# Kernel tuning notes

Hardware: AMD Instinct MI355X
Metric: run time of the kernel (lower is better)

The kernel has to match this reference:

```python
import jax, jax.numpy as jnp
import numpy as np

N = 100_000   # nodes
E = 3_200_000 # edges (avg degree 32)

def _glorot(k, shape):
    fan_in, fan_out = shape
    lim = float(np.sqrt(6.0 / (fan_in + fan_out)))
    return jax.random.uniform(k, shape, jnp.float32, -lim, lim)

def setup_inputs() -> dict:
    key = jax.random.key(0)
    ks = jax.random.split(key, 8)
    x = jax.random.normal(ks[0], (N, 3), dtype=jnp.float32)
    edge_index = jax.random.randint(ks[1], (2, E), 0, N, dtype=jnp.int32)
    choices = jax.random.bernoulli(ks[2], 0.5, (N,))
    W1 = _glorot(ks[3], (3, 16));  b1 = jnp.zeros((16,), jnp.float32)
    W2 = _glorot(ks[4], (16, 16)); b2 = jnp.zeros((16,), jnp.float32)
    W3 = _glorot(ks[5], (16, 1));  b3 = jnp.zeros((1,), jnp.float32)
    fc_w = _glorot(ks[6], (16, 1)); fc_b = jnp.zeros((1,), jnp.float32)
    return dict(x=x, edge_index=edge_index, choices=choices,
                W1=W1, b1=b1, W2=W2, b2=b2, W3=W3, b3=b3,
                fc_w=fc_w, fc_b=fc_b)

def reference(x, edge_index, choices, W1, b1, W2, b2, W3, b3, fc_w, fc_b):
    row, col = edge_index[0], edge_index[1]  # source -> target
    # improved=True GCN norm: self-loop weight 2, deg = in_degree + 2
    deg = jax.ops.segment_sum(jnp.ones((E,), x.dtype), col, num_segments=N) + 2.0
    dinv = jax.lax.rsqrt(deg)                    # [N]
    enorm = dinv[row] * dinv[col]                # [E] edge normalization
    self_norm = 2.0 * dinv * dinv                # [N] self-loop term

    def gcn(h, W, b):
        h = h @ W                                # [N, F_out]
        agg = jax.ops.segment_sum(h[row] * enorm[:, None], col, num_segments=N)
        return agg + self_norm[:, None] * h + b

    h = jax.nn.relu(gcn(x, W1, b1))
    h = jax.nn.relu(gcn(h, W2, b2))
    c = gcn(h, W3, b3)[:, 0]                     # [N] per-node logit
    # masked softmax over chosen nodes (torch masked_select + softmax,
    # expressed with static shape: non-chosen entries get probability 0)
    logits = jnp.where(choices, c, -jnp.inf)
    choice = jax.nn.softmax(logits, axis=0)      # [N]
    # global_mean_pool with a single graph = mean over all nodes
    v = jnp.mean(h, axis=0, keepdims=True)       # [1, 16]
    value = v @ fc_w + fc_b                      # [1, 1]
    return choice, value
```

## Files before the change

### kernel.cpp

```cpp
#include <hip/hip_runtime.h>
#include <hip/hip_fp16.h>
#include <math.h>

#define BLK 256


#define BSH 8
#define NB 512
#define CAP 10240
#define SCAP 12288
#define EB 8192
#define BINTH 1024

__device__ inline float4 load_h4(const __half* base, int node, int sub) {
    const uint2* p = reinterpret_cast<const uint2*>(base + ((size_t)node << 4)) + sub;
    uint2 u = *p;
    union { unsigned u; __half2 h; } a, b;
    a.u = u.x; b.u = u.y;
    float2 fa = __half22float2(a.h), fb = __half22float2(b.h);
    return make_float4(fa.x, fa.y, fb.x, fb.y);
}

__device__ inline void store_h4(__half* base, int node, int sub, float4 v) {
    union { unsigned u; __half2 h; } a, b;
    a.h = __floats2half2_rn(v.x, v.y);
    b.h = __floats2half2_rn(v.z, v.w);
    uint2 u; u.x = a.u; u.y = b.u;
    *(reinterpret_cast<uint2*>(base + ((size_t)node << 4)) + sub) = u;
}

__device__ inline float3 load_xs(const __half* xs, int node) {
    uint2 u = *reinterpret_cast<const uint2*>(xs + ((size_t)node << 2));
    union { unsigned u; __half2 h; } a, b;
    a.u = u.x; b.u = u.y;
    float2 fa = __half22float2(a.h), fb = __half22float2(b.h);
    return make_float3(fa.x, fa.y, fb.x);
}

__global__ void k_init(int* __restrict__ gcur, float* __restrict__ scal) {
    int t = threadIdx.x;
    gcur[t] = 0;
    if (t < 18) scal[t] = 0.f;
}

__global__ void __launch_bounds__(BINTH) k_bin(const int* __restrict__ row,
                                               const int* __restrict__ col,
                                               int* __restrict__ gcur,
                                               int* __restrict__ packed, int E) {
    __shared__ int stage[EB];
    __shared__ unsigned short sbuk[EB];
    __shared__ int hist[NB];
    __shared__ int lscan[NB];
    __shared__ int cur[NB];
    __shared__ int gbase[NB];
    int tid = threadIdx.x;
    int base = blockIdx.x * EB;
    int cnt = min(EB, E - base);

    if (tid < NB) hist[tid] = 0;
    __syncthreads();
    for (int j = tid; j < cnt; j += BINTH) {
        int c = __builtin_nontemporal_load(col + base + j);
        atomicAdd(&hist[c >> BSH], 1);
    }
    __syncthreads();
    if (tid < NB) lscan[tid] = hist[tid];
    __syncthreads();
    for (int d = 1; d < NB; d <<= 1) {
        int t = (tid < NB && tid >= d) ? lscan[tid - d] : 0;
        __syncthreads();
        if (tid < NB && tid >= d) lscan[tid] += t;
        __syncthreads();
    }
    if (tid < NB) {
        int ex = lscan[tid] - hist[tid];
        lscan[tid] = ex;
        cur[tid] = ex;
    }
    __syncthreads();
    for (int j = tid; j < cnt; j += BINTH) {
        int c = __builtin_nontemporal_load(col + base + j);
        int r = __builtin_nontemporal_load(row + base + j);
        int b = c >> BSH;
        int p = atomicAdd(&cur[b], 1);
        stage[p] = (r << BSH) | (c & ((1 << BSH) - 1));
        sbuk[p] = (unsigned short)b;
    }
    __syncthreads();
    if (tid < NB && hist[tid] > 0)
        gbase[tid] = tid * CAP + atomicAdd(&gcur[tid], hist[tid]);
    __syncthreads();
    for (int j = tid; j < cnt; j += BINTH) {
        int b = sbuk[j];
        int pos = gbase[b] + (j - lscan[b]);
        packed[pos] = stage[j];
    }
}

__global__ void __launch_bounds__(BLK) k_place(const int* __restrict__ packed,
                                               const int* __restrict__ bcnt,
                                               const float* __restrict__ x,
                                               int* __restrict__ degi,
                                               int* __restrict__ offs,
                                               float* __restrict__ dinv,
                                               __half* __restrict__ xs,
                                               int* __restrict__ srcs, int n) {
    __shared__ int cnt[256];
    __shared__ int lcur[256];
    __shared__ int ssum[256];
    __shared__ int stg[SCAP];
    int tid = threadIdx.x;
    int b = blockIdx.x;
    int nb0 = b << BSH;
    cnt[tid] = 0;
    __syncthreads();
    int ecnt = bcnt[b];
    const int* pk = packed + (size_t)b * CAP;
    for (int j = tid; j < ecnt; j += BLK)
        atomicAdd(&cnt[pk[j] & 255], 1);
    __syncthreads();
    int c = cnt[tid];
    int pl = (c + 7) & ~7;
    ssum[tid] = pl;
    __syncthreads();
    for (int d = 1; d < 256; d <<= 1) {
        int t = (tid >= d) ? ssum[tid - d] : 0;
        __syncthreads();
        if (tid >= d) ssum[tid] += t;
        __syncthreads();
    }
    int Arel = ssum[tid] - pl;
    lcur[tid] = Arel;
    int A = b * SCAP + Arel;
    int valid = min(n - nb0, 256);
    int i = nb0 + tid;
    if (tid < valid) {
        degi[i] = pl;
        offs[i] = A;
        float di = rsqrtf((float)c + 2.0f);
        dinv[i] = di;
        float x0 = x[i * 3 + 0], x1 = x[i * 3 + 1], x2 = x[i * 3 + 2];
        union { unsigned u; __half2 h; } a2, b2;
        a2.h = __floats2half2_rn(di * x0, di * x1);
        b2.h = __floats2half2_rn(di * x2, 0.f);
        uint2 u; u.x = a2.u; u.y = b2.u;
        *reinterpret_cast<uint2*>(xs + ((size_t)i << 2)) = u;
        for (int k = c; k < pl; k++) stg[Arel + k] = n;
    }
    if (b == 0 && tid == 0) {
        uint2 z; z.x = 0u; z.y = 0u;
        *reinterpret_cast<uint2*>(xs + ((size_t)n << 2)) = z;
    }
    __syncthreads();
    for (int j = tid; j < ecnt; j += BLK) {
        int v = pk[j];
        int slot = atomicAdd(&lcur[v & 255], 1);
        stg[slot] = v >> BSH;
    }
    __syncthreads();
    int total = ssum[255];
    int gb = b * SCAP;
    for (int j = tid; j < total; j += BLK)
        srcs[gb + j] = stg[j];
}

__global__ void __launch_bounds__(BLK) k_agg1(const __half* __restrict__ xs,
                                              const int* __restrict__ offs,
                                              const int* __restrict__ degi,
                                              const int* __restrict__ srcs,
                                              const float* __restrict__ dinv,
                                              const float* __restrict__ b1,
                                              const float* __restrict__ W1,
                                              const float* __restrict__ W2,
                                              __half* __restrict__ hwsB, int n) {
    __shared__ float w1[48];
    __shared__ float w2[256];
    __shared__ float bb[16];
    __shared__ float hbuf[64][17];
    int tid = threadIdx.x;
    w2[tid] = W2[tid];
    if (tid < 48) w1[tid] = W1[tid];
    if (tid < 16) bb[tid] = b1[tid];
    if (blockIdx.x == 0 && tid < 8)
        reinterpret_cast<unsigned*>(hwsB + ((size_t)n << 4))[tid] = 0u;
    __syncthreads();
    int t = tid >> 2, sub = tid & 3;
    int i = blockIdx.x * 64 + t;
    bool act = (i < n);
    int A  = act ? offs[i] : 0;
    int pl = act ? degi[i] : 0;
    int o = 4 * sub;
    int clamp = max(pl - 4, 0);
    float ax0 = 0.f, ay0 = 0.f, az0 = 0.f;
    float ax1 = 0.f, ay1 = 0.f, az1 = 0.f;
    for (int j = 0; j < pl; j += 32) {
        int i0 = j + o;
        int i1 = j + 16 + o;
        int ja = min(i0, clamp);
        int jb = min(i1, clamp);
        int4 sa = *reinterpret_cast<const int4*>(srcs + A + ja);
        int4 sb = *reinterpret_cast<const int4*>(srcs + A + jb);
        if (i0 >= pl) sa = make_int4(n, n, n, n);
        if (i1 >= pl) sb = make_int4(n, n, n, n);
        float3 qa0 = load_xs(xs, sa.x);
        float3 qa1 = load_xs(xs, sa.y);
        float3 qa2 = load_xs(xs, sa.z);
        float3 qa3 = load_xs(xs, sa.w);
        float3 qb0 = load_xs(xs, sb.x);
        float3 qb1 = load_xs(xs, sb.y);
        float3 qb2 = load_xs(xs, sb.z);
        float3 qb3 = load_xs(xs, sb.w);
        ax0 += qa0.x + qa1.x + qa2.x + qa3.x;
        ay0 += qa0.y + qa1.y + qa2.y + qa3.y;
        az0 += qa0.z + qa1.z + qa2.z + qa3.z;
        ax1 += qb0.x + qb1.x + qb2.x + qb3.x;
        ay1 += qb0.y + qb1.y + qb2.y + qb3.y;
        az1 += qb0.z + qb1.z + qb2.z + qb3.z;
    }
    float ax = ax0 + ax1, ay = ay0 + ay1, az = az0 + az1;
    ax += __shfl_xor(ax, 1); ay += __shfl_xor(ay, 1); az += __shfl_xor(az, 1);
    ax += __shfl_xor(ax, 2); ay += __shfl_xor(ay, 2); az += __shfl_xor(az, 2);
    float di = 0.f;
    if (act) {
        di = dinv[i];
        float3 s = load_xs(xs, i);
        float axs = ax + 2.f * s.x, ays = ay + 2.f * s.y, azs = az + 2.f * s.z;
#pragma unroll
        for (int k = 0; k < 4; k++) {
            int f = sub * 4 + k;
            float hv = di * (axs * w1[f] + ays * w1[16 + f] + azs * w1[32 + f]) + bb[f];
            hbuf[t][f] = fmaxf(hv, 0.f);
        }
    }
    __syncthreads();
    if (act) {
        const float* hn = hbuf[t];
        float s0 = 0.f, s1 = 0.f, s2 = 0.f, s3 = 0.f;
#pragma unroll
        for (int f = 0; f < 16; f++) {
            float hv = hn[f];
            const float4 wq = *(const float4*)&w2[f * 16 + sub * 4];
            s0 += hv * wq.x; s1 += hv * wq.y; s2 += hv * wq.z; s3 += hv * wq.w;
        }
        store_h4(hwsB, i, sub, make_float4(di * s0, di * s1, di * s2, di * s3));
    }
}

__global__ void __launch_bounds__(BLK) k_agg2(const __half* __restrict__ hwsB,
                                              const int* __restrict__ offs,
                                              const int* __restrict__ degi,
                                              const int* __restrict__ srcs,
                                              const float* __restrict__ dinv,
                                              const float* __restrict__ b2,
                                              const float* __restrict__ W3,
                                              float* __restrict__ hws3,
                                              float* __restrict__ pool, int n) {
    __shared__ float w3[16];
    __shared__ float bb[16];
    __shared__ float lp[16];
    int tid = threadIdx.x;
    if (tid < 16) { w3[tid] = W3[tid]; bb[tid] = b2[tid]; lp[tid] = 0.f; }
    if (blockIdx.x == 0 && tid == 0) hws3[n] = 0.f;
    __syncthreads();
    int t = tid >> 2, sub = tid & 3;
    int i = blockIdx.x * 64 + t;
    bool act = (i < n);
    float di = act ? dinv[i] : 0.f;
    int A  = act ? offs[i] : 0;
    int pl = act ? degi[i] : 0;
    float4 z4 = make_float4(0.f, 0.f, 0.f, 0.f);
    float4 s = act ? load_h4(hwsB, i, sub) : z4;
    float4 acc0 = make_float4(2.f * s.x, 2.f * s.y, 2.f * s.z, 2.f * s.w);
    float4 acc1 = z4, acc2 = z4, acc3 = z4;
    int clamp8 = max(pl - 8, 0);
    for (int j = 0; j < pl; j += 16) {
        int j1 = j + 8;
        int jb = min(j1, clamp8);
        int4 sa0 = *reinterpret_cast<const int4*>(srcs + A + j);
        int4 sa1 = *reinterpret_cast<const int4*>(srcs + A + j + 4);
        int4 sb0 = *reinterpret_cast<const int4*>(srcs + A + jb);
        int4 sb1 = *reinterpret_cast<const int4*>(srcs + A + jb + 4);
        if (j1 >= pl) { sb0 = make_int4(n, n, n, n); sb1 = sb0; }
        float4 qa0 = load_h4(hwsB, sa0.x, sub);
        float4 qa1 = load_h4(hwsB, sa0.y, sub);
        float4 qa2 = load_h4(hwsB, sa0.z, sub);
        float4 qa3 = load_h4(hwsB, sa0.w, sub);
        float4 qa4 = load_h4(hwsB, sa1.x, sub);
        float4 qa5 = load_h4(hwsB, sa1.y, sub);
        float4 qa6 = load_h4(hwsB, sa1.z, sub);
        float4 qa7 = load_h4(hwsB, sa1.w, sub);
        float4 qb0 = load_h4(hwsB, sb0.x, sub);
        float4 qb1 = load_h4(hwsB, sb0.y, sub);
        float4 qb2 = load_h4(hwsB, sb0.z, sub);
        float4 qb3 = load_h4(hwsB, sb0.w, sub);
        float4 qb4 = load_h4(hwsB, sb1.x, sub);
        float4 qb5 = load_h4(hwsB, sb1.y, sub);
        float4 qb6 = load_h4(hwsB, sb1.z, sub);
        float4 qb7 = load_h4(hwsB, sb1.w, sub);
        acc0.x += qa0.x + qa2.x + qa4.x + qa6.x;
        acc0.y += qa0.y + qa2.y + qa4.y + qa6.y;
        acc0.z += qa0.z + qa2.z + qa4.z + qa6.z;
        acc0.w += qa0.w + qa2.w + qa4.w + qa6.w;
        acc1.x += qa1.x + qa3.x + qa5.x + qa7.x;
        acc1.y += qa1.y + qa3.y + qa5.y + qa7.y;
        acc1.z += qa1.z + qa3.z + qa5.z + qa7.z;
        acc1.w += qa1.w + qa3.w + qa5.w + qa7.w;
        acc2.x += qb0.x + qb2.x + qb4.x + qb6.x;
        acc2.y += qb0.y + qb2.y + qb4.y + qb6.y;
        acc2.z += qb0.z + qb2.z + qb4.z + qb6.z;
        acc2.w += qb0.w + qb2.w + qb4.w + qb6.w;
        acc3.x += qb1.x + qb3.x + qb5.x + qb7.x;
        acc3.y += qb1.y + qb3.y + qb5.y + qb7.y;
        acc3.z += qb1.z + qb3.z + qb5.z + qb7.z;
        acc3.w += qb1.w + qb3.w + qb5.w + qb7.w;
    }
    acc0.x += acc1.x + acc2.x + acc3.x;
    acc0.y += acc1.y + acc2.y + acc3.y;
    acc0.z += acc1.z + acc2.z + acc3.z;
    acc0.w += acc1.w + acc2.w + acc3.w;
    float4 hA = z4;
    if (act) {
        hA.x = fmaxf(di * acc0.x + bb[sub * 4 + 0], 0.f);
        hA.y = fmaxf(di * acc0.y + bb[sub * 4 + 1], 0.f);
        hA.z = fmaxf(di * acc0.z + bb[sub * 4 + 2], 0.f);
        hA.w = fmaxf(di * acc0.w + bb[sub * 4 + 3], 0.f);
    }
    float pA = hA.x * w3[sub * 4 + 0] + hA.y * w3[sub * 4 + 1]
             + hA.z * w3[sub * 4 + 2] + hA.w * w3[sub * 4 + 3];
    pA += __shfl_xor(pA, 1); pA += __shfl_xor(pA, 2);
    if (sub == 0 && act) hws3[i] = di * pA;
    float4 hp = hA;
#pragma unroll
    for (int m = 4; m < 64; m <<= 1) {
        hp.x += __shfl_xor(hp.x, m);
        hp.y += __shfl_xor(hp.y, m);
        hp.z += __shfl_xor(hp.z, m);
        hp.w += __shfl_xor(hp.w, m);
    }
    if ((tid & 63) < 4) {
        atomicAdd(&lp[sub * 4 + 0], hp.x);
        atomicAdd(&lp[sub * 4 + 1], hp.y);
        atomicAdd(&lp[sub * 4 + 2], hp.z);
        atomicAdd(&lp[sub * 4 + 3], hp.w);
    }
    __syncthreads();
    if (tid < 16) atomicAdd(&pool[tid], lp[tid]);
}

__global__ void __launch_bounds__(BLK) k_agg3(const float* __restrict__ hws3,
                                              const int* __restrict__ offs,
                                              const int* __restrict__ degi,
                                              const int* __restrict__ srcs,
                                              const float* __restrict__ dinv,
                                              const float* __restrict__ b3,
                                              const int* __restrict__ choices,
                                              float* __restrict__ cbuf,
                                              float* __restrict__ bmax,
                                              float* __restrict__ bsum, int n) {
    __shared__ float red[BLK];
    int tid = threadIdx.x;
    int nl = tid >> 2, sub = tid & 3;
    int iA = blockIdx.x * 128 + nl;
    int iB = iA + 64;
    bool actA = (iA < n), actB = (iB < n);
    int AA = actA ? offs[iA] : 0;
    int AB = actB ? offs[iB] : 0;
    int plA = actA ? degi[iA] : 0;
    int plB = actB ? degi[iB] : 0;
    float sA0 = 0.f, sA1 = 0.f, sB0 = 0.f, sB1 = 0.f;
    int plM = max(plA, plB);
    for (int j = 8 * sub; j < plM; j += 32) {
        int ja = min(j, max(plA - 8, 0));
        int jb = min(j, max(plB - 8, 0));
        int4 sa0 = *reinterpret_cast<const int4*>(srcs + AA + ja);
        int4 sa1 = *reinterpret_cast<const int4*>(srcs + AA + ja + 4);
        int4 sb0 = *reinterpret_cast<const int4*>(srcs + AB + jb);
        int4 sb1 = *reinterpret_cast<const int4*>(srcs + AB + jb + 4);
        if (j >= plA) { sa0 = make_int4(n, n, n, n); sa1 = sa0; }
        if (j >= plB) { sb0 = make_int4(n, n, n, n); sb1 = sb0; }
        sA0 += hws3[sa0.x] + hws3[sa0.z] + hws3[sa1.x] + hws3[sa1.z];
        sA1 += hws3[sa0.y] + hws3[sa0.w] + hws3[sa1.y] + hws3[sa1.w];
        sB0 += hws3[sb0.x] + hws3[sb0.z] + hws3[sb1.x] + hws3[sb1.z];
        sB1 += hws3[sb0.y] + hws3[sb0.w] + hws3[sb1.y] + hws3[sb1.w];
    }
    float sA = sA0 + sA1, sB = sB0 + sB1;
    sA += __shfl_xor(sA, 1); sA += __shfl_xor(sA, 2);
    sB += __shfl_xor(sB, 1); sB += __shfl_xor(sB, 2);
    float lA = -INFINITY, lB = -INFINITY;
    if (sub == 0) {
        if (actA) {
            float c = dinv[iA] * (sA + 2.f * hws3[iA]) + b3[0];
            cbuf[iA] = c;
            if (choices[iA] != 0) lA = c;
        }
        if (actB) {
            float c = dinv[iB] * (sB + 2.f * hws3[iB]) + b3[0];
            cbuf[iB] = c;
            if (choices[iB] != 0) lB = c;
        }
    }
    red[tid] = fmaxf(lA, lB);
    __syncthreads();
    for (int d = BLK / 2; d > 0; d >>= 1) {
        if (tid < d) red[tid] = fmaxf(red[tid], red[tid + d]);
        __syncthreads();
    }
    float bm = red[0];
    __syncthreads();
    float es = 0.f;
    if (lA > -INFINITY) es += expf(lA - bm);
    if (lB > -INFINITY) es += expf(lB - bm);
    red[tid] = es;
    __syncthreads();
    for (int d = BLK / 2; d > 0; d >>= 1) {
        if (tid < d) red[tid] += red[tid + d];
        __syncthreads();
    }
    if (tid == 0) { bmax[blockIdx.x] = bm; bsum[blockIdx.x] = red[0]; }
}

__global__ void __launch_bounds__(BLK) k_final(const float* __restrict__ cbuf,
                                               const int* __restrict__ choices,
                                               const float* __restrict__ bmax,
                                               const float* __restrict__ bsum,
                                               const float* __restrict__ pool,
                                               const float* __restrict__ fcw,
                                               const float* __restrict__ fcb,
                                               float* __restrict__ out,
                                               int nblk, int n) {
    __shared__ float red[BLK];
    __shared__ float MS[2];
    int tid = threadIdx.x;
    float m = -INFINITY;
    for (int i = tid; i < nblk; i += BLK) m = fmaxf(m, bmax[i]);
    red[tid] = m;
    __syncthreads();
    for (int d = BLK / 2; d > 0; d >>= 1) {
        if (tid < d) red[tid] = fmaxf(red[tid], red[tid + d]);
        __syncthreads();
    }
    float M = red[0];
    __syncthreads();
    float s = 0.f;
    for (int i = tid; i < nblk; i += BLK) {
        float bm = bmax[i];
        if (bm > -INFINITY) s += bsum[i] * expf(bm - M);
    }
    red[tid] = s;
    __syncthreads();
    for (int d = BLK / 2; d > 0; d >>= 1) {
        if (tid < d) red[tid] += red[tid + d];
        __syncthreads();
    }
    if (tid == 0) { MS[0] = M; MS[1] = red[0]; }
    __syncthreads();
    float Mv = MS[0], Sv = MS[1];
    int i = blockIdx.x * BLK + tid;
    if (i < n) {
        float p = 0.0f;
        if (choices[i] != 0) p = expf(cbuf[i] - Mv) / Sv;
        out[i] = p;
    }
    if (blockIdx.x == 0 && tid == 0) {
        float invn = 1.0f / (float)n;
        float v = 0.0f;
#pragma unroll
        for (int f = 0; f < 16; f++) v += (pool[f] * invn) * fcw[f];
        out[n] = v + fcb[0];
    }
}

extern "C" void kernel_launch(void* const* d_in, const int* in_sizes, int n_in,
                              void* d_out, int out_size, void* d_ws, size_t ws_size,
                              hipStream_t stream) {
    const float* x       = (const float*)d_in[0];
    const int*   ei      = (const int*)d_in[1];
    const int*   choices = (const int*)d_in[2];
    const float* W1 = (const float*)d_in[3];
    const float* b1 = (const float*)d_in[4];
    const float* W2 = (const float*)d_in[5];
    const float* b2 = (const float*)d_in[6];
    const float* W3 = (const float*)d_in[7];
    const float* b3 = (const float*)d_in[8];
    const float* fcw = (const float*)d_in[9];
    const float* fcb = (const float*)d_in[10];
    float* out = (float*)d_out;

    int n = in_sizes[0] / 3;
    int E = in_sizes[1] / 2;
    const int* row = ei;
    const int* col = ei + E;

    int nblkN = (n + BLK - 1) / BLK;
    int nblk64 = (n + 63) / 64;
    int nblk128 = (n + 127) / 128;
    int nbuck = (n + (1 << BSH) - 1) >> BSH;
    int nblkBin = (E + EB - 1) / EB;

    char* ws = (char*)d_ws;
    size_t o = 0;
    auto alloc = [&](size_t bytes) { char* p = ws + o; o += (bytes + 15) & ~(size_t)15; return p; };
    int*   degi   = (int*)  alloc((size_t)n * 4);
    int*   offs   = (int*)  alloc((size_t)n * 4);
    float* dinv   = (float*)alloc((size_t)n * 4);
    float* hws3   = (float*)alloc((size_t)(n + 1) * 4);
    float* cbuf   = (float*)alloc((size_t)n * 4);
    float* bmax   = (float*)alloc(8192);
    float* bsum   = (float*)alloc(8192);
    int*   gcur   = (int*)  alloc(NB * 4);
    float* scal   = (float*)alloc(256);
    float* pool   = scal + 1;
    __half* xs    = (__half*)alloc((size_t)(n + 1) * 4 * 2);
    size_t hw_bytes = (size_t)(n + 1) * 16 * 2;
    size_t pk_bytes = (size_t)NB * CAP * 4;
    char*  blob   = alloc(hw_bytes > pk_bytes ? hw_bytes : pk_bytes);
    int*    packed = (int*)blob;
    __half* hwsB   = (__half*)blob;
    int*   srcs   = (int*)  alloc((size_t)NB * SCAP * 4);
    (void)ws_size;

    k_init<<<1, NB, 0, stream>>>(gcur, scal);
    k_bin<<<nblkBin, BINTH, 0, stream>>>(row, col, gcur, packed, E);
    k_place<<<nbuck, BLK, 0, stream>>>(packed, gcur, x, degi, offs, dinv, xs, srcs, n);

    k_agg1<<<nblk64, BLK, 0, stream>>>(xs, offs, degi, srcs, dinv, b1, W1, W2, hwsB, n);
    k_agg2<<<nblk64, BLK, 0, stream>>>(hwsB, offs, degi, srcs, dinv, b2, W3, hws3, pool, n);
    k_agg3<<<nblk128, BLK, 0, stream>>>(hws3, offs, degi, srcs, dinv, b3, choices, cbuf, bmax, bsum, n);

    k_final<<<nblkN, BLK, 0, stream>>>(cbuf, choices, bmax, bsum, pool, fcw, fcb, out, nblk128, n);
}
```

Measured before the change: 210.5 us.

## Sort nodes by padded degree within buckets to balance aggregation wavefronts

In the placement kernel, each 256-node bucket builds a permutation that groups nodes by padded degree class using a small shared-memory counting sort. The three aggregation kernels read node ids through this permutation, so wavefronts handle nodes of similar degree and spend fewer iterations on idle lanes. The cost is an extra perm array, one more indirection per node, and less contiguous access to per-node arrays. Grid sizes now come from the bucket count, and padded slots map to the dummy node n.

Result: slower. 218.5 us (+3.8%).

```diff
diff --git a/kernel.cpp b/kernel.cpp
--- a/kernel.cpp
+++ b/kernel.cpp
@@ -104,15 +104,19 @@
                                                int* __restrict__ offs,
                                                float* __restrict__ dinv,
                                                __half* __restrict__ xs,
-                                               int* __restrict__ srcs, int n) {
+                                               int* __restrict__ srcs,
+                                               int* __restrict__ perm, int n) {
     __shared__ int cnt[256];
     __shared__ int lcur[256];
     __shared__ int ssum[256];
+    __shared__ int h2[34];
+    __shared__ int b2s[34];
     __shared__ int stg[SCAP];
     int tid = threadIdx.x;
     int b = blockIdx.x;
     int nb0 = b << BSH;
     cnt[tid] = 0;
+    if (tid < 34) h2[tid] = 0;
     __syncthreads();
     int ecnt = bcnt[b];
     const int* pk = packed + (size_t)b * CAP;
@@ -134,16 +138,26 @@
     int A = b * SCAP + Arel;
     int valid = min(n - nb0, 256);
     int i = nb0 + tid;
+    int key = (tid < valid) ? min(pl >> 3, 31) : 32;
+    atomicAdd(&h2[key], 1);
+    __syncthreads();
+    if (tid == 0) {
+        int s = 0;
+        for (int k = 0; k < 33; k++) { b2s[k] = s; s += h2[k]; }
+    }
+    __syncthreads();
+    int rank = atomicAdd(&b2s[key], 1);
+    perm[(b << 8) + rank] = (tid < valid) ? i : n;
     if (tid < valid) {
         degi[i] = pl;
         offs[i] = A;
         float di = rsqrtf((float)c + 2.0f);
         dinv[i] = di;
         float x0 = x[i * 3 + 0], x1 = x[i * 3 + 1], x2 = x[i * 3 + 2];
-        union { unsigned u; __half2 h; } a2, b2;
+        union { unsigned u; __half2 h; } a2, b2u;
         a2.h = __floats2half2_rn(di * x0, di * x1);
-        b2.h = __floats2half2_rn(di * x2, 0.f);
-        uint2 u; u.x = a2.u; u.y = b2.u;
+        b2u.h = __floats2half2_rn(di * x2, 0.f);
+        uint2 u; u.x = a2.u; u.y = b2u.u;
         *reinterpret_cast<uint2*>(xs + ((size_t)i << 2)) = u;
         for (int k = c; k < pl; k++) stg[Arel + k] = n;
     }
@@ -169,6 +183,7 @@
                                               const int* __restrict__ degi,
                                               const int* __restrict__ srcs,
                                               const float* __restrict__ dinv,
+                                              const int* __restrict__ perm,
                                               const float* __restrict__ b1,
                                               const float* __restrict__ W1,
                                               const float* __restrict__ W2,
@@ -185,7 +200,7 @@
         reinterpret_cast<unsigned*>(hwsB + ((size_t)n << 4))[tid] = 0u;
     __syncthreads();
     int t = tid >> 2, sub = tid & 3;
-    int i = blockIdx.x * 64 + t;
+    int i = perm[blockIdx.x * 64 + t];
     bool act = (i < n);
     int A  = act ? offs[i] : 0;
     int pl = act ? degi[i] : 0;
@@ -251,6 +266,7 @@
                                               const int* __restrict__ degi,
                                               const int* __restrict__ srcs,
                                               const float* __restrict__ dinv,
+                                              const int* __restrict__ perm,
                                               const float* __restrict__ b2,
                                               const float* __restrict__ W3,
                                               float* __restrict__ hws3,
@@ -263,7 +279,7 @@
     if (blockIdx.x == 0 && tid == 0) hws3[n] = 0.f;
     __syncthreads();
     int t = tid >> 2, sub = tid & 3;
-    int i = blockIdx.x * 64 + t;
+    int i = perm[blockIdx.x * 64 + t];
     bool act = (i < n);
     float di = act ? dinv[i] : 0.f;
     int A  = act ? offs[i] : 0;
@@ -352,6 +368,7 @@
                                               const int* __restrict__ degi,
                                               const int* __restrict__ srcs,
                                               const float* __restrict__ dinv,
+                                              const int* __restrict__ perm,
                                               const float* __restrict__ b3,
                                               const int* __restrict__ choices,
                                               float* __restrict__ cbuf,
@@ -360,8 +377,8 @@
     __shared__ float red[BLK];
     int tid = threadIdx.x;
     int nl = tid >> 2, sub = tid & 3;
-    int iA = blockIdx.x * 128 + nl;
-    int iB = iA + 64;
+    int iA = perm[blockIdx.x * 128 + nl];
+    int iB = perm[blockIdx.x * 128 + 64 + nl];
     bool actA = (iA < n), actB = (iB < n);
     int AA = actA ? offs[iA] : 0;
     int AB = actB ? offs[iB] : 0;
@@ -492,9 +509,9 @@
     const int* col = ei + E;
 
     int nblkN = (n + BLK - 1) / BLK;
-    int nblk64 = (n + 63) / 64;
-    int nblk128 = (n + 127) / 128;
     int nbuck = (n + (1 << BSH) - 1) >> BSH;
+    int nblk64 = nbuck * 4;
+    int nblk128 = nbuck * 2;
     int nblkBin = (E + EB - 1) / EB;
 
     char* ws = (char*)d_ws;
@@ -510,6 +527,7 @@
     int*   gcur   = (int*)  alloc(NB * 4);
     float* scal   = (float*)alloc(256);
     float* pool   = scal + 1;
+    int*   perm   = (int*)  alloc((size_t)NB * 256 * 4);
     __half* xs    = (__half*)alloc((size_t)(n + 1) * 4 * 2);
     size_t hw_bytes = (size_t)(n + 1) * 16 * 2;
     size_t pk_bytes = (size_t)NB * CAP * 4;
@@ -521,11 +539,11 @@
 
     k_init<<<1, NB, 0, stream>>>(gcur, scal);
     k_bin<<<nblkBin, BINTH, 0, stream>>>(row, col, gcur, packed, E);
-    k_place<<<nbuck, BLK, 0, stream>>>(packed, gcur, x, degi, offs, dinv, xs, srcs, n);
-
-    k_agg1<<<nblk64, BLK, 0, stream>>>(xs, offs, degi, srcs, dinv, b1, W1, W2, hwsB, n);
-    k_agg2<<<nblk64, BLK, 0, stream>>>(hwsB, offs, degi, srcs, dinv, b2, W3, hws3, pool, n);
-    k_agg3<<<nblk128, BLK, 0, stream>>>(hws3, offs, degi, srcs, dinv, b3, choices, cbuf, bmax, bsum, n);
+    k_place<<<nbuck, BLK, 0, stream>>>(packed, gcur, x, degi, offs, dinv, xs, srcs, perm, n);
+
+    k_agg1<<<nblk64, BLK, 0, stream>>>(xs, offs, degi, srcs, dinv, perm, b1, W1, W2, hwsB, n);
+    k_agg2<<<nblk64, BLK, 0, stream>>>(hwsB, offs, degi, srcs, dinv, perm, b2, W3, hws3, pool, n);
+    k_agg3<<<nblk128, BLK, 0, stream>>>(hws3, offs, degi, srcs, dinv, perm, b3, choices, cbuf, bmax, bsum, n);
 
     k_final<<<nblkN, BLK, 0, stream>>>(cbuf, choices, bmax, bsum, pool, fcw, fcb, out, nblk128, n);
 }
```
